# Performance work log

Measured on AMD Instinct MI355X. Metric: run time of the kernel, lower is better.

Reference implementation:

```python
import jax, jax.numpy as jnp
import numpy as np

VOCAB = 50257
DIM = 1024
B, S = 8, 4096


def setup_inputs() -> dict:
    key = jax.random.key(0)
    kw, kx = jax.random.split(key)
    # Materialize a float source table, then quantize exactly as BNB8bitEmbedding.__init__:
    # per-row absmax (+1e-8), scale to [-127,127], round, clamp, cast to int8.
    w = jax.random.normal(kw, (VOCAB, DIM), dtype=jnp.float32)
    absmax = jnp.abs(w).max(axis=1) + 1e-8                      # [VOCAB]
    q_weight = jnp.clip(jnp.round(w / absmax[:, None] * 127.0), -128, 127).astype(jnp.int8)
    x = jax.random.randint(kx, (B, S), 0, VOCAB, dtype=jnp.int32)
    return {"x": x, "q_weight": q_weight, "absmax": absmax}


def reference(x, q_weight, absmax) -> jnp.ndarray:
    # Fused equivalent of the chunked masked-scatter loop: since absmax is per-row,
    # the chunk partition is a no-op mathematically -> single gather + dequant.
    scale = absmax[x] * (1.0 / 127.0)                            # [B, S]
    return q_weight[x].astype(jnp.float32) * scale[..., None]    # [B, S, DIM]
```

## Files before the change

kernel.cpp:

```cpp
#include <hip/hip_runtime.h>


__global__ __launch_bounds__(256) void bnb8_embed_kernel(
    const int* __restrict__ x,
    const int* __restrict__ qw,
    const float* __restrict__ absmax,
    float* __restrict__ out,
    int dim)
{
    const int t = blockIdx.x;
    const int row = x[t];
    const float scale = absmax[row] * (1.0f / 127.0f);

    const int i = threadIdx.x << 2;
    const size_t row_off = (size_t)row * (size_t)dim + i;
    const size_t out_off = (size_t)t * (size_t)dim + i;

    const int4 q = *(const int4*)(qw + row_off);

    float4 o;
    o.x = (float)q.x * scale;
    o.y = (float)q.y * scale;
    o.z = (float)q.z * scale;
    o.w = (float)q.w * scale;

    *(float4*)(out + out_off) = o;
}

extern "C" void kernel_launch(void* const* d_in, const int* in_sizes, int n_in,
                              void* d_out, int out_size, void* d_ws, size_t ws_size,
                              hipStream_t stream) {
    const int*   x      = (const int*)d_in[0];
    const int*   qw     = (const int*)d_in[1];
    const float* absmax = (const float*)d_in[2];
    float*       out    = (float*)d_out;

    const int n_tokens = in_sizes[0];
    const int dim = out_size / n_tokens;
    const int threads = dim / 4;

    bnb8_embed_kernel<<<n_tokens, threads, 0, stream>>>(x, qw, absmax, out, dim);
}
```

Before: 304.1 us.

## Process eight tokens per block with batched loads and nontemporal stores

Each block now handles eight tokens instead of one. All eight row indices, scales and weight vectors are loaded before any output is written, which raises memory-level parallelism and cuts the block count by eight. Output writes use nontemporal stores so the large streaming output does not pollute cache. This assumes the token count is divisible by eight and increases register use per thread.

```diff
diff --git a/kernel.cpp b/kernel.cpp
--- a/kernel.cpp
+++ b/kernel.cpp
@@ -1,30 +1,47 @@
 #include <hip/hip_runtime.h>
 
+
+#define TOKS 8
+
+typedef float v4f __attribute__((ext_vector_type(4)));
+typedef int   v4i __attribute__((ext_vector_type(4)));
 
 __global__ __launch_bounds__(256) void bnb8_embed_kernel(
     const int* __restrict__ x,
     const int* __restrict__ qw,
     const float* __restrict__ absmax,
     float* __restrict__ out,
+    int n_tokens,
     int dim)
 {
-    const int t = blockIdx.x;
-    const int row = x[t];
-    const float scale = absmax[row] * (1.0f / 127.0f);
+    const int t0 = blockIdx.x * TOKS;
+    const int e = threadIdx.x << 2;
 
-    const int i = threadIdx.x << 2;
-    const size_t row_off = (size_t)row * (size_t)dim + i;
-    const size_t out_off = (size_t)t * (size_t)dim + i;
+    int rows[TOKS];
+#pragma unroll
+    for (int j = 0; j < TOKS; ++j)
+        rows[j] = x[t0 + j];
 
-    const int4 q = *(const int4*)(qw + row_off);
+    float scale[TOKS];
+#pragma unroll
+    for (int j = 0; j < TOKS; ++j)
+        scale[j] = absmax[rows[j]] * (1.0f / 127.0f);
 
-    float4 o;
-    o.x = (float)q.x * scale;
-    o.y = (float)q.y * scale;
-    o.z = (float)q.z * scale;
-    o.w = (float)q.w * scale;
+    v4i q[TOKS];
+#pragma unroll
+    for (int j = 0; j < TOKS; ++j)
+        q[j] = *(const v4i*)(qw + (size_t)rows[j] * (size_t)dim + e);
 
-    *(float4*)(out + out_off) = o;
+#pragma unroll
+    for (int j = 0; j < TOKS; ++j) {
+        v4f o;
+        o.x = (float)q[j].x * scale[j];
+        o.y = (float)q[j].y * scale[j];
+        o.z = (float)q[j].z * scale[j];
+        o.w = (float)q[j].w * scale[j];
+        v4f* dst = (v4f*)(out + (size_t)(t0 + j) * (size_t)dim + e);
+        __builtin_nontemporal_store(o, dst);
+    }
 }
 
 extern "C" void kernel_launch(void* const* d_in, const int* in_sizes, int n_in,
@@ -38,6 +55,8 @@
     const int n_tokens = in_sizes[0];
     const int dim = out_size / n_tokens;
     const int threads = dim / 4;
+    const int blocks = n_tokens / TOKS;
 
-    bnb8_embed_kernel<<<n_tokens, threads, 0, stream>>>(x, qw, absmax, out, dim);
+    bnb8_embed_kernel<<<blocks, threads, 0, stream>>>(x, qw, absmax, out,
+                                                      n_tokens, dim);
 }
```

Result: no change. 304.6 us (+0.1%).
